# Kernel tuning notes

Hardware: AMD Instinct MI355X
Metric: run time of the kernel (lower is better)

## Reference

```python
import jax, jax.numpy as jnp
import numpy as np

B, S, D, H = 2, 2048, 1024, 16
DK = D // H  # 64
THETA = 10000.0


def setup_inputs() -> dict:
    key = jax.random.key(0)
    ks = jax.random.split(key, 5)
    std = float(np.sqrt(2.0 / (D + D)))
    x = jax.random.normal(ks[0], (B, S, D), dtype=jnp.float32)
    q_proj = jax.random.normal(ks[1], (D, D), dtype=jnp.float32) * std
    k_proj = jax.random.normal(ks[2], (D, D), dtype=jnp.float32) * std
    v_proj = jax.random.normal(ks[3], (D, D), dtype=jnp.float32) * std
    o_proj = jax.random.normal(ks[4], (D, D), dtype=jnp.float32) * std
    token_positions = jnp.arange(S, dtype=jnp.int32).reshape(1, S)
    return {"x": x, "token_positions": token_positions,
            "q_proj": q_proj, "k_proj": k_proj, "v_proj": v_proj, "o_proj": o_proj}


def _rope(t, pos):
    # t: [B, H, S, DK]; pos: [S]. Equivalent to multiplying by the block-diagonal
    # rotation matrix R[pos] in the source (interleaved 2x2 rotations).
    inv_freq = 1.0 / (THETA ** (2.0 * jnp.arange(DK // 2, dtype=jnp.float32) / DK))
    ang = pos.astype(jnp.float32)[:, None] * inv_freq[None, :]  # [S, DK/2]
    c, s = jnp.cos(ang), jnp.sin(ang)
    t0, t1 = t[..., 0::2], t[..., 1::2]
    out0 = c * t0 - s * t1
    out1 = s * t0 + c * t1
    return jnp.stack([out0, out1], axis=-1).reshape(t.shape)


def reference(x, token_positions, q_proj, k_proj, v_proj, o_proj):
    def split_heads(t):  # [B,S,D] -> [B,H,S,DK]
        return t.reshape(B, S, H, DK).transpose(0, 2, 1, 3)

    q = split_heads(jnp.einsum('bsd,ed->bse', x, q_proj))
    k = split_heads(jnp.einsum('bsd,ed->bse', x, k_proj))
    v = split_heads(jnp.einsum('bsd,ed->bse', x, v_proj))

    pos = token_positions[0]
    q = _rope(q, pos)
    k = _rope(k, pos)

    scores = jnp.einsum('bhqd,bhkd->bhqk', q, k) / jnp.sqrt(jnp.float32(DK))
    causal = jnp.tril(jnp.ones((S, S), dtype=bool))
    scores = jnp.where(causal, scores, -jnp.inf)

    # Faithful to source softmax: subtract the GLOBAL max (x.max()), then row-normalize.
    p = jnp.exp(scores - jnp.max(scores))
    p = p / jnp.sum(p, axis=-1, keepdims=True)

    attn = jnp.einsum('bhqk,bhkd->bhqd', p, v)
    attn = attn.transpose(0, 2, 1, 3).reshape(B, S, D)  # merge heads
    return jnp.einsum('bsd,ed->bse', attn, o_proj)
```

## Files before the change

kernel.cpp:

```cpp
#include <hip/hip_runtime.h>
#include <math.h>

#define B_  2
#define S_  2048
#define D_  1024
#define H_  16
#define DK_ 64
#define M_  (B_ * S_)

using u16 = unsigned short;
using u32 = unsigned int;
typedef __attribute__((ext_vector_type(8))) short  short8;
typedef __attribute__((ext_vector_type(4))) short  short4v;
typedef __attribute__((ext_vector_type(4))) float  float4v;
typedef __attribute__((ext_vector_type(4))) float  f32x4;

__device__ __forceinline__ float bf2f(u16 h) {
  u32 u = ((u32)h) << 16;
  return __builtin_bit_cast(float, u);
}
__device__ __forceinline__ u16 f2bf(float f) {
  u32 u = __builtin_bit_cast(u32, f);
  u32 r = u + 0x7fffu + ((u >> 16) & 1u);
  return (u16)(r >> 16);
}
__device__ __forceinline__ u16 f2bf_fast(float f) {
  u32 u = __builtin_bit_cast(u32, f);
  return (u16)((u + 0x8000u) >> 16);
}

__device__ __forceinline__ void async16(const void* g, void* l) {
  __builtin_amdgcn_global_load_lds((const __attribute__((address_space(1))) void*)g,
                                   (__attribute__((address_space(3))) void*)l,
                                   16, 0, 0);
}

#define MFMA16(a, b, c) __builtin_amdgcn_mfma_f32_16x16x32_bf16((a), (b), (c), 0, 0, 0)

__device__ __forceinline__ void stc(u16* p, float v)   { *p = f2bf(v); }
__device__ __forceinline__ void stc(float* p, float v) { *p = v; }

#define XG_ (M_ * D_ / 4)
#define WG_ (D_ * D_ / 4)
__global__ __launch_bounds__(256) void cvt5_kernel(
    const float* __restrict__ x,  const float* __restrict__ wq,
    const float* __restrict__ wk, const float* __restrict__ wv,
    const float* __restrict__ wo, u16* __restrict__ Xb, u16* __restrict__ Wqb,
    u16* __restrict__ Wkb, u16* __restrict__ Wvb, u16* __restrict__ Wob) {
  int i = blockIdx.x * 256 + threadIdx.x;
  const float* s; u16* d; int off;
  if (i < XG_)                { s = x;  d = Xb;  off = i; }
  else if (i < XG_ + WG_)     { s = wq; d = Wqb; off = i - XG_; }
  else if (i < XG_ + 2 * WG_) { s = wk; d = Wkb; off = i - XG_ - WG_; }
  else if (i < XG_ + 3 * WG_) { s = wv; d = Wvb; off = i - XG_ - 2 * WG_; }
  else                        { s = wo; d = Wob; off = i - XG_ - 3 * WG_; }
  f32x4 v = ((const f32x4*)s)[off];
  short4v o;
  o[0] = (short)f2bf(v[0]); o[1] = (short)f2bf(v[1]);
  o[2] = (short)f2bf(v[2]); o[3] = (short)f2bf(v[3]);
  ((short4v*)d)[off] = o;
}

template <typename TC>
__device__ __forceinline__ void gemm_tile(const u16* __restrict__ A,
                                          const u16* __restrict__ Bw,
                                          TC* __restrict__ C,
                                          int K, int N, int m0, int n0) {
  __shared__ __align__(16) u16 As[128 * 32];
  __shared__ __align__(16) u16 Bs[128 * 32];
  const int tid  = threadIdx.x;
  const int lane = tid & 63;
  const int wave = tid >> 6;
  const int quad = lane >> 4;
  const int l15  = lane & 15;
  const int wm   = (wave >> 1) << 6;
  const int wn   = (wave & 1) << 6;

  float4v acc[4][4];
#pragma unroll
  for (int i = 0; i < 4; ++i)
#pragma unroll
    for (int j = 0; j < 4; ++j) acc[i][j] = (float4v){0.f, 0.f, 0.f, 0.f};

  for (int k0 = 0; k0 < K; k0 += 32) {
#pragma unroll
    for (int i = 0; i < 2; ++i) {
      const int cbase = i * 256 + wave * 64;
      const int c     = cbase + lane;
      async16(A  + (size_t)(m0 + (c >> 2)) * K + k0 + ((c & 3) << 3), As + cbase * 8);
      async16(Bw + (size_t)(n0 + (c >> 2)) * K + k0 + ((c & 3) << 3), Bs + cbase * 8);
    }
    __syncthreads();

    short8 af[4], bfr[4];
#pragma unroll
    for (int mi = 0; mi < 4; ++mi)
      af[mi] = *(const short8*)(As + (wm + mi * 16 + l15) * 32 + quad * 8);
#pragma unroll
    for (int ni = 0; ni < 4; ++ni)
      bfr[ni] = *(const short8*)(Bs + (wn + ni * 16 + l15) * 32 + quad * 8);
#pragma unroll
    for (int mi = 0; mi < 4; ++mi)
#pragma unroll
      for (int ni = 0; ni < 4; ++ni)
        acc[mi][ni] = MFMA16(af[mi], bfr[ni], acc[mi][ni]);
    __syncthreads();
  }

#pragma unroll
  for (int mi = 0; mi < 4; ++mi)
#pragma unroll
    for (int ni = 0; ni < 4; ++ni)
#pragma unroll
      for (int r = 0; r < 4; ++r) {
        const int row = m0 + wm + mi * 16 + quad * 4 + r;
        const int col = n0 + wn + ni * 16 + l15;
        stc(C + (size_t)row * N + col, acc[mi][ni][r]);
      }
}

__global__ __launch_bounds__(256) void gemm_qkv_kernel(
    const u16* __restrict__ X, const u16* __restrict__ Wq,
    const u16* __restrict__ Wk, const u16* __restrict__ Wv,
    u16* Qb, u16* Kb, u16* Vb) {
  const int mt  = blockIdx.x;
  const int nn  = blockIdx.y;
  const int sel = nn >> 3;
  const int nt  = nn & 7;
  const u16* Bw = (sel == 0) ? Wq : (sel == 1) ? Wk : Wv;
  u16*       C  = (sel == 0) ? Qb : (sel == 1) ? Kb : Vb;
  gemm_tile(X, Bw, C, D_, D_, mt * 128, nt * 128);
}

__global__ __launch_bounds__(256) void gemm_o_kernel(
    const u16* __restrict__ Ab, const u16* __restrict__ Wo, float* Out) {
  gemm_tile(Ab, Wo, Out, D_, D_, blockIdx.x * 128, blockIdx.y * 128);
}

__global__ void rope_kernel(u16* __restrict__ Qb, u16* __restrict__ Kb,
                            const void* __restrict__ posv) {
  const int idx = blockIdx.x * 256 + threadIdx.x;
  const int i = idx & 31;
  const int h = (idx >> 5) & (H_ - 1);
  const int s = (idx >> 9) & (S_ - 1);
  const int b = idx >> 20;
  const int* p32 = (const int*)posv;
  const bool is64 = (p32[1] == 0 && p32[2] == 1);
  const int  ps   = is64 ? p32[2 * s] : p32[s];
  const float p    = (float)ps;
  const float freq = exp2f(-0.4152410118609203f * (float)i);
  float sn, cs;
  sincosf(p * freq, &sn, &cs);
  const size_t base = (size_t)(b * S_ + s) * D_ + h * DK_ + 2 * i;
  const float q0v = bf2f(Qb[base]), q1v = bf2f(Qb[base + 1]);
  Qb[base]     = f2bf(0.125f * (cs * q0v - sn * q1v));
  Qb[base + 1] = f2bf(0.125f * (sn * q0v + cs * q1v));
  const float k0v = bf2f(Kb[base]), k1v = bf2f(Kb[base + 1]);
  Kb[base]     = f2bf(cs * k0v - sn * k1v);
  Kb[base + 1] = f2bf(sn * k0v + cs * k1v);
}

__global__ __launch_bounds__(256) void vtrans_kernel(const u16* __restrict__ Vb,
                                                     u16* __restrict__ Vt) {
  const int sblk = blockIdx.x;
  const int bh   = blockIdx.y;
  const int b = bh >> 4, h = bh & 15;
  const int t = threadIdx.x;
  const int s0 = sblk * 64;
  __shared__ __align__(16) u16 T[64 * 72];

  {
    const int srow = t >> 2;
    const int dseg = (t & 3) << 4;
    const u16* g = Vb + (size_t)(b * S_ + s0 + srow) * D_ + h * DK_ + dseg;
    *(short8*)(T + srow * 72 + dseg)     = *(const short8*)(g);
    *(short8*)(T + srow * 72 + dseg + 8) = *(const short8*)(g + 8);
  }
  __syncthreads();
  {
    const int dk   = t >> 2;
    const int sseg = (t & 3) << 4;
    short8 o0, o1;
#pragma unroll
    for (int j = 0; j < 8; ++j) {
      o0[j] = (short)T[(sseg + j) * 72 + dk];
      o1[j] = (short)T[(sseg + 8 + j) * 72 + dk];
    }
    u16* g = Vt + (size_t)(bh * DK_ + dk) * S_ + s0 + sseg;
    *(short8*)(g)     = o0;
    *(short8*)(g + 8) = o1;
  }
}

__global__ __launch_bounds__(128) void attn_kernel(const u16* __restrict__ Qb,
                                                   const u16* __restrict__ Kb,
                                                   const u16* __restrict__ Vt,
                                                   u16* __restrict__ Ob) {
  const int qt = (blockIdx.x + blockIdx.y) & 31;
  const int bh = blockIdx.y;
  const int b = bh >> 4, h = bh & 15;
  const int tid = threadIdx.x, lane = tid & 63, wave = tid >> 6;
  const int quad = lane >> 4, l15 = lane & 15;
  const int qw = qt * 64 + wave * 32;

  __shared__ __align__(16) u16 Ks[2][64 * 64];
  __shared__ __align__(16) u16 Vs[2][64 * 64];

  const u16* Kbh = Kb + (size_t)b * S_ * D_ + h * DK_;
  const u16* Vbh = Vt + (size_t)bh * DK_ * S_;

  auto stage = [&](int kt, int bsel) {
    const int k0 = kt * 64;
#pragma unroll
    for (int i = 0; i < 4; ++i) {
      const int cb  = i * 128 + wave * 64;
      const int c   = cb + lane;
      const int row = c >> 3;
      const int gch = (c & 7) ^ (row & 7);
      async16(Kbh + (size_t)(k0 + row) * D_ + gch * 8, &Ks[bsel][cb * 8]);
      async16(Vbh + (size_t)row * S_ + k0 + gch * 8, &Vs[bsel][cb * 8]);
    }
  };

  short8 qf[2][2];
#pragma unroll
  for (int rg = 0; rg < 2; ++rg) {
    const u16* qrow = Qb + (size_t)(b * S_ + qw + rg * 16 + l15) * D_ + h * DK_;
    qf[rg][0] = *(const short8*)(qrow + quad * 8);
    qf[rg][1] = *(const short8*)(qrow + 32 + quad * 8);
  }

  float4v oacc[2][4];
#pragma unroll
  for (int rg = 0; rg < 2; ++rg)
#pragma unroll
    for (int n2 = 0; n2 < 4; ++n2) oacc[rg][n2] = (float4v){0.f, 0.f, 0.f, 0.f};
  float lsum0 = 0.f, lsum1 = 0.f;

  stage(0, 0);

  for (int kt = 0; kt <= qt; ++kt) {
    const int bsel = kt & 1;
    __syncthreads();
    if (kt < qt) stage(kt + 1, bsel ^ 1);

    const u16* ks = Ks[bsel];
    const u16* vs = Vs[bsel];

    float4v sc[2][4];
#pragma unroll
    for (int ni = 0; ni < 4; ++ni) {
      const int kr = ni * 16 + l15;
      const int x  = kr & 7;
      const short8 kf0 = *(const short8*)(ks + kr * 64 + ((quad ^ x) << 3));
      const short8 kf1 = *(const short8*)(ks + kr * 64 + (((quad | 4) ^ x) << 3));
      float4v z = (float4v){0.f, 0.f, 0.f, 0.f};
      sc[0][ni] = MFMA16(kf1, qf[0][1], MFMA16(kf0, qf[0][0], z));
      sc[1][ni] = MFMA16(kf1, qf[1][1], MFMA16(kf0, qf[1][0], z));
    }

    const int k0 = kt * 64;
    if (kt == qt) {
#pragma unroll
      for (int rg = 0; rg < 2; ++rg) {
        const int qr = qw + rg * 16 + l15;
#pragma unroll
        for (int ni = 0; ni < 4; ++ni)
#pragma unroll
          for (int r = 0; r < 4; ++r) {
            const float e = __expf(sc[rg][ni][r]);
            sc[rg][ni][r] = (k0 + ni * 16 + quad * 4 + r > qr) ? 0.f : e;
          }
      }
    } else {
#pragma unroll
      for (int rg = 0; rg < 2; ++rg)
#pragma unroll
        for (int ni = 0; ni < 4; ++ni)
#pragma unroll
          for (int r = 0; r < 4; ++r) sc[rg][ni][r] = __expf(sc[rg][ni][r]);
    }

    short8 pfr[2][2];
#pragma unroll
    for (int rg = 0; rg < 2; ++rg)
#pragma unroll
      for (int s = 0; s < 2; ++s) {
        short8 pf;
#pragma unroll
        for (int r = 0; r < 4; ++r) {
          pf[r]     = (short)f2bf_fast(sc[rg][2 * s][r]);
          pf[r + 4] = (short)f2bf_fast(sc[rg][2 * s + 1][r]);
        }
        pfr[rg][s] = pf;
      }
#pragma unroll
    for (int ni = 0; ni < 4; ++ni)
#pragma unroll
      for (int r = 0; r < 4; ++r) {
        lsum0 += sc[0][ni][r];
        lsum1 += sc[1][ni][r];
      }

#pragma unroll
    for (int s = 0; s < 2; ++s)
#pragma unroll
      for (int n2 = 0; n2 < 4; ++n2) {
        const int vr = n2 * 16 + l15;
        const int x  = vr & 7;
        const int cl = (((s << 2) | (quad >> 1)) ^ x);
        const int ch = (((s << 2) | 2 | (quad >> 1)) ^ x);
        const int hb = (quad & 1) << 2;
        short4v vlo = *(const short4v*)(vs + vr * 64 + (cl << 3) + hb);
        short4v vhi = *(const short4v*)(vs + vr * 64 + (ch << 3) + hb);
        short8 vf;
#pragma unroll
        for (int e = 0; e < 4; ++e) { vf[e] = vlo[e]; vf[e + 4] = vhi[e]; }
        oacc[0][n2] = MFMA16(pfr[0][s], vf, oacc[0][n2]);
        oacc[1][n2] = MFMA16(pfr[1][s], vf, oacc[1][n2]);
      }
  }

  float ls[2] = {lsum0, lsum1};
#pragma unroll
  for (int rg = 0; rg < 2; ++rg) {
    float t = ls[rg];
    t += __shfl_xor(t, 16, 64);
    t += __shfl_xor(t, 32, 64);
    float rinv[4];
#pragma unroll
    for (int r = 0; r < 4; ++r) rinv[r] = 1.0f / __shfl(t, quad * 4 + r, 64);
#pragma unroll
    for (int n2 = 0; n2 < 4; ++n2)
#pragma unroll
      for (int r = 0; r < 4; ++r) {
        const int srow = qw + rg * 16 + quad * 4 + r;
        Ob[(size_t)(b * S_ + srow) * D_ + h * DK_ + n2 * 16 + l15] =
            f2bf(oacc[rg][n2][r] * rinv[r]);
      }
  }
}

extern "C" void kernel_launch(void* const* d_in, const int* in_sizes, int n_in,
                              void* d_out, int out_size, void* d_ws, size_t ws_size,
                              hipStream_t stream) {
  const float* x  = (const float*)d_in[0];
  const void*  tp = d_in[1];
  const float* wq = (const float*)d_in[2];
  const float* wk = (const float*)d_in[3];
  const float* wv = (const float*)d_in[4];
  const float* wo = (const float*)d_in[5];
  float* out = (float*)d_out;

  u16* Qb  = (u16*)d_ws;
  u16* Kb  = Qb + (size_t)M_ * D_;
  u16* Vb  = Kb + (size_t)M_ * D_;
  u16* Vt  = Vb + (size_t)M_ * D_;
  u16* Ab  = Vt + (size_t)M_ * D_;
  u16* Xb  = Ab;
  u16* Wqb = Ab + (size_t)M_ * D_;
  u16* Wkb = Wqb + (size_t)D_ * D_;
  u16* Wvb = Wkb + (size_t)D_ * D_;
  u16* Wob = Wvb + (size_t)D_ * D_;

  cvt5_kernel<<<dim3((XG_ + 4 * WG_) / 256), dim3(256), 0, stream>>>(
      x, wq, wk, wv, wo, Xb, Wqb, Wkb, Wvb, Wob);
  gemm_qkv_kernel<<<dim3(32, 24), dim3(256), 0, stream>>>(Xb, Wqb, Wkb, Wvb, Qb, Kb, Vb);
  rope_kernel<<<dim3((B_ * S_ * H_ * 32) / 256), dim3(256), 0, stream>>>(Qb, Kb, tp);
  vtrans_kernel<<<dim3(32, 32), dim3(256), 0, stream>>>(Vb, Vt);
  attn_kernel<<<dim3(32, 32), dim3(128), 0, stream>>>(Qb, Kb, Vt, Ab);
  gemm_o_kernel<<<dim3(32, 8), dim3(256), 0, stream>>>(Ab, Wob, out);
}
```

Before: 211.9 us.

## Deepen attention K/V pipeline with half-tiles, vectorize RoPE, reorder query tiles

The attention kernel now streams K/V in 32-key half-tiles through a 4-slot LDS ring with three loads in flight and explicit vmcnt waits instead of a double buffer with __syncthreads. It also sets wave priority around the MFMA sections, packs probabilities with v_cvt_pk_bf16_f32, and remaps query tiles so short and long causal rows are interleaved. The RoPE kernel processes 8 elements per thread with 16-byte loads and stores instead of scalar accesses. The aim is to hide load latency and cut conversion and memory-instruction overhead. In exchange, the kernel uses hand-written waitcnt counts that must match the number of issued loads, and each half-tile does fewer MFMAs per barrier.

```diff
diff --git a/kernel.cpp b/kernel.cpp
--- a/kernel.cpp
+++ b/kernel.cpp
@@ -14,6 +14,7 @@
 typedef __attribute__((ext_vector_type(4))) short  short4v;
 typedef __attribute__((ext_vector_type(4))) float  float4v;
 typedef __attribute__((ext_vector_type(4))) float  f32x4;
+typedef __attribute__((ext_vector_type(4))) u32    u32x4;
 
 __device__ __forceinline__ float bf2f(u16 h) {
   u32 u = ((u32)h) << 16;
@@ -23,10 +24,6 @@
   u32 u = __builtin_bit_cast(u32, f);
   u32 r = u + 0x7fffu + ((u >> 16) & 1u);
   return (u16)(r >> 16);
-}
-__device__ __forceinline__ u16 f2bf_fast(float f) {
-  u32 u = __builtin_bit_cast(u32, f);
-  return (u16)((u + 0x8000u) >> 16);
 }
 
 __device__ __forceinline__ void async16(const void* g, void* l) {
@@ -137,27 +134,37 @@
   gemm_tile(Ab, Wo, Out, D_, D_, blockIdx.x * 128, blockIdx.y * 128);
 }
 
-__global__ void rope_kernel(u16* __restrict__ Qb, u16* __restrict__ Kb,
-                            const void* __restrict__ posv) {
-  const int idx = blockIdx.x * 256 + threadIdx.x;
-  const int i = idx & 31;
-  const int h = (idx >> 5) & (H_ - 1);
-  const int s = (idx >> 9) & (S_ - 1);
-  const int b = idx >> 20;
+__global__ __launch_bounds__(256) void rope_kernel(u16* __restrict__ Qb,
+                                                   u16* __restrict__ Kb,
+                                                   const void* __restrict__ posv) {
+  const int t  = blockIdx.x * 256 + threadIdx.x;
+  const int p4 = t & 7;
+  const int h  = (t >> 3) & (H_ - 1);
+  const int s  = (t >> 7) & (S_ - 1);
+  const int b  = t >> 18;
   const int* p32 = (const int*)posv;
   const bool is64 = (p32[1] == 0 && p32[2] == 1);
   const int  ps   = is64 ? p32[2 * s] : p32[s];
-  const float p    = (float)ps;
-  const float freq = exp2f(-0.4152410118609203f * (float)i);
-  float sn, cs;
-  sincosf(p * freq, &sn, &cs);
-  const size_t base = (size_t)(b * S_ + s) * D_ + h * DK_ + 2 * i;
-  const float q0v = bf2f(Qb[base]), q1v = bf2f(Qb[base + 1]);
-  Qb[base]     = f2bf(0.125f * (cs * q0v - sn * q1v));
-  Qb[base + 1] = f2bf(0.125f * (sn * q0v + cs * q1v));
-  const float k0v = bf2f(Kb[base]), k1v = bf2f(Kb[base + 1]);
-  Kb[base]     = f2bf(cs * k0v - sn * k1v);
-  Kb[base + 1] = f2bf(sn * k0v + cs * k1v);
+  const float p   = (float)ps;
+  const size_t base = (size_t)(b * S_ + s) * D_ + h * DK_ + p4 * 8;
+  short8 qv = *(const short8*)(Qb + base);
+  short8 kv = *(const short8*)(Kb + base);
+  short8 qo, ko;
+#pragma unroll
+  for (int j = 0; j < 4; ++j) {
+    const int i = p4 * 4 + j;
+    const float freq = exp2f(-0.4152410118609203f * (float)i);
+    float sn, cs;
+    sincosf(p * freq, &sn, &cs);
+    const float q0v = bf2f((u16)qv[2 * j]), q1v = bf2f((u16)qv[2 * j + 1]);
+    qo[2 * j]     = (short)f2bf(0.125f * (cs * q0v - sn * q1v));
+    qo[2 * j + 1] = (short)f2bf(0.125f * (sn * q0v + cs * q1v));
+    const float k0v = bf2f((u16)kv[2 * j]), k1v = bf2f((u16)kv[2 * j + 1]);
+    ko[2 * j]     = (short)f2bf(cs * k0v - sn * k1v);
+    ko[2 * j + 1] = (short)f2bf(sn * k0v + cs * k1v);
+  }
+  *(short8*)(Qb + base) = qo;
+  *(short8*)(Kb + base) = ko;
 }
 
 __global__ __launch_bounds__(256) void vtrans_kernel(const u16* __restrict__ Vb,
@@ -196,29 +203,39 @@
                                                    const u16* __restrict__ Kb,
                                                    const u16* __restrict__ Vt,
                                                    u16* __restrict__ Ob) {
-  const int qt = (blockIdx.x + blockIdx.y) & 31;
+  const int j5 = (blockIdx.x + blockIdx.y) & 31;
+  const int r5 = j5 & 7, g5 = j5 >> 3;
+  const int qt = (g5 == 0) ? r5 : (g5 == 1) ? r5 + 8 : (g5 == 2) ? 23 - r5 : 31 - r5;
   const int bh = blockIdx.y;
   const int b = bh >> 4, h = bh & 15;
   const int tid = threadIdx.x, lane = tid & 63, wave = tid >> 6;
   const int quad = lane >> 4, l15 = lane & 15;
   const int qw = qt * 64 + wave * 32;
 
-  __shared__ __align__(16) u16 Ks[2][64 * 64];
-  __shared__ __align__(16) u16 Vs[2][64 * 64];
+  __shared__ __align__(16) u16 Kh[4][32 * 64];
+  __shared__ __align__(16) u16 Vh[4][64 * 32];
 
   const u16* Kbh = Kb + (size_t)b * S_ * D_ + h * DK_;
   const u16* Vbh = Vt + (size_t)bh * DK_ * S_;
 
-  auto stage = [&](int kt, int bsel) {
-    const int k0 = kt * 64;
-#pragma unroll
-    for (int i = 0; i < 4; ++i) {
-      const int cb  = i * 128 + wave * 64;
+  auto stage = [&](int j) {
+    const int sel = j & 3;
+    const int k0  = j * 32;
+#pragma unroll
+    for (int i = 0; i < 2; ++i) {
+      const int cb  = wave * 128 + i * 64;
       const int c   = cb + lane;
       const int row = c >> 3;
-      const int gch = (c & 7) ^ (row & 7);
-      async16(Kbh + (size_t)(k0 + row) * D_ + gch * 8, &Ks[bsel][cb * 8]);
-      async16(Vbh + (size_t)row * S_ + k0 + gch * 8, &Vs[bsel][cb * 8]);
+      const int ch  = (c & 7) ^ (row & 7);
+      async16(Kbh + (size_t)(k0 + row) * D_ + ch * 8, &Kh[sel][cb * 8]);
+    }
+#pragma unroll
+    for (int i = 0; i < 2; ++i) {
+      const int cb = wave * 128 + i * 64;
+      const int c  = cb + lane;
+      const int rv = c >> 2;
+      const int ch = (c & 3) ^ ((rv >> 1) & 3);
+      async16(Vbh + (size_t)rv * S_ + k0 + ch * 8, &Vh[sel][cb * 8]);
     }
   };
 
@@ -237,19 +254,27 @@
     for (int n2 = 0; n2 < 4; ++n2) oacc[rg][n2] = (float4v){0.f, 0.f, 0.f, 0.f};
   float lsum0 = 0.f, lsum1 = 0.f;
 
-  stage(0, 0);
-
-  for (int kt = 0; kt <= qt; ++kt) {
-    const int bsel = kt & 1;
-    __syncthreads();
-    if (kt < qt) stage(kt + 1, bsel ^ 1);
-
-    const u16* ks = Ks[bsel];
-    const u16* vs = Vs[bsel];
-
-    float4v sc[2][4];
-#pragma unroll
-    for (int ni = 0; ni < 4; ++ni) {
+  const int NS = 2 * qt + 2;
+  stage(0);
+  stage(1);
+  if (NS > 2) stage(2);
+
+  for (int hs = 0; hs < NS; ++hs) {
+    if (hs + 2 < NS)      asm volatile("s_waitcnt vmcnt(8)" ::: "memory");
+    else if (hs + 1 < NS) asm volatile("s_waitcnt vmcnt(4)" ::: "memory");
+    else                  asm volatile("s_waitcnt vmcnt(0)" ::: "memory");
+    __builtin_amdgcn_s_barrier();
+    asm volatile("" ::: "memory");
+    if (hs + 3 < NS) stage(hs + 3);
+
+    const int sel = hs & 3;
+    const u16* ks = Kh[sel];
+    const u16* vs = Vh[sel];
+
+    float4v sc[2][2];
+    __builtin_amdgcn_s_setprio(1);
+#pragma unroll
+    for (int ni = 0; ni < 2; ++ni) {
       const int kr = ni * 16 + l15;
       const int x  = kr & 7;
       const short8 kf0 = *(const short8*)(ks + kr * 64 + ((quad ^ x) << 3));
@@ -258,67 +283,63 @@
       sc[0][ni] = MFMA16(kf1, qf[0][1], MFMA16(kf0, qf[0][0], z));
       sc[1][ni] = MFMA16(kf1, qf[1][1], MFMA16(kf0, qf[1][0], z));
     }
-
-    const int k0 = kt * 64;
-    if (kt == qt) {
+    __builtin_amdgcn_s_setprio(0);
+
+    const int kbase = hs * 32;
+    if (kbase + 31 > qw) {
 #pragma unroll
       for (int rg = 0; rg < 2; ++rg) {
         const int qr = qw + rg * 16 + l15;
 #pragma unroll
-        for (int ni = 0; ni < 4; ++ni)
+        for (int ni = 0; ni < 2; ++ni)
 #pragma unroll
           for (int r = 0; r < 4; ++r) {
             const float e = __expf(sc[rg][ni][r]);
-            sc[rg][ni][r] = (k0 + ni * 16 + quad * 4 + r > qr) ? 0.f : e;
+            sc[rg][ni][r] = (kbase + ni * 16 + quad * 4 + r > qr) ? 0.f : e;
           }
       }
     } else {
 #pragma unroll
       for (int rg = 0; rg < 2; ++rg)
 #pragma unroll
-        for (int ni = 0; ni < 4; ++ni)
+        for (int ni = 0; ni < 2; ++ni)
 #pragma unroll
           for (int r = 0; r < 4; ++r) sc[rg][ni][r] = __expf(sc[rg][ni][r]);
     }
 
-    short8 pfr[2][2];
-#pragma unroll
-    for (int rg = 0; rg < 2; ++rg)
-#pragma unroll
-      for (int s = 0; s < 2; ++s) {
-        short8 pf;
-#pragma unroll
-        for (int r = 0; r < 4; ++r) {
-          pf[r]     = (short)f2bf_fast(sc[rg][2 * s][r]);
-          pf[r + 4] = (short)f2bf_fast(sc[rg][2 * s + 1][r]);
-        }
-        pfr[rg][s] = pf;
-      }
-#pragma unroll
-    for (int ni = 0; ni < 4; ++ni)
+    short8 pfr[2];
+#pragma unroll
+    for (int rg = 0; rg < 2; ++rg) {
+      u32 w0, w1, w2, w3;
+      asm("v_cvt_pk_bf16_f32 %0, %1, %2" : "=v"(w0) : "v"(sc[rg][0][0]), "v"(sc[rg][0][1]));
+      asm("v_cvt_pk_bf16_f32 %0, %1, %2" : "=v"(w1) : "v"(sc[rg][0][2]), "v"(sc[rg][0][3]));
+      asm("v_cvt_pk_bf16_f32 %0, %1, %2" : "=v"(w2) : "v"(sc[rg][1][0]), "v"(sc[rg][1][1]));
+      asm("v_cvt_pk_bf16_f32 %0, %1, %2" : "=v"(w3) : "v"(sc[rg][1][2]), "v"(sc[rg][1][3]));
+      u32x4 ww = (u32x4){w0, w1, w2, w3};
+      pfr[rg] = __builtin_bit_cast(short8, ww);
+    }
+#pragma unroll
+    for (int ni = 0; ni < 2; ++ni)
 #pragma unroll
       for (int r = 0; r < 4; ++r) {
         lsum0 += sc[0][ni][r];
         lsum1 += sc[1][ni][r];
       }
 
-#pragma unroll
-    for (int s = 0; s < 2; ++s)
-#pragma unroll
-      for (int n2 = 0; n2 < 4; ++n2) {
-        const int vr = n2 * 16 + l15;
-        const int x  = vr & 7;
-        const int cl = (((s << 2) | (quad >> 1)) ^ x);
-        const int ch = (((s << 2) | 2 | (quad >> 1)) ^ x);
-        const int hb = (quad & 1) << 2;
-        short4v vlo = *(const short4v*)(vs + vr * 64 + (cl << 3) + hb);
-        short4v vhi = *(const short4v*)(vs + vr * 64 + (ch << 3) + hb);
-        short8 vf;
-#pragma unroll
-        for (int e = 0; e < 4; ++e) { vf[e] = vlo[e]; vf[e + 4] = vhi[e]; }
-        oacc[0][n2] = MFMA16(pfr[0][s], vf, oacc[0][n2]);
-        oacc[1][n2] = MFMA16(pfr[1][s], vf, oacc[1][n2]);
-      }
+    __builtin_amdgcn_s_setprio(1);
+#pragma unroll
+    for (int n2 = 0; n2 < 4; ++n2) {
+      const int vr = n2 * 16 + l15;
+      const int sw = (vr >> 1) & 3;
+      const short4v vlo = *(const short4v*)(vs + vr * 32 + (((quad >> 1) ^ sw) << 3) + ((quad & 1) << 2));
+      const short4v vhi = *(const short4v*)(vs + vr * 32 + (((2 | (quad >> 1)) ^ sw) << 3) + ((quad & 1) << 2));
+      short8 vf;
+#pragma unroll
+      for (int e = 0; e < 4; ++e) { vf[e] = vlo[e]; vf[e + 4] = vhi[e]; }
+      oacc[0][n2] = MFMA16(pfr[0], vf, oacc[0][n2]);
+      oacc[1][n2] = MFMA16(pfr[1], vf, oacc[1][n2]);
+    }
+    __builtin_amdgcn_s_setprio(0);
   }
 
   float ls[2] = {lsum0, lsum1};
@@ -366,7 +387,7 @@
   cvt5_kernel<<<dim3((XG_ + 4 * WG_) / 256), dim3(256), 0, stream>>>(
       x, wq, wk, wv, wo, Xb, Wqb, Wkb, Wvb, Wob);
   gemm_qkv_kernel<<<dim3(32, 24), dim3(256), 0, stream>>>(Xb, Wqb, Wkb, Wvb, Qb, Kb, Vb);
-  rope_kernel<<<dim3((B_ * S_ * H_ * 32) / 256), dim3(256), 0, stream>>>(Qb, Kb, tp);
+  rope_kernel<<<dim3((B_ * S_ * H_ * 8) / 256), dim3(256), 0, stream>>>(Qb, Kb, tp);
   vtrans_kernel<<<dim3(32, 32), dim3(256), 0, stream>>>(Vb, Vt);
   attn_kernel<<<dim3(32, 32), dim3(128), 0, stream>>>(Qb, Kb, Vt, Ab);
   gemm_o_kernel<<<dim3(32, 8), dim3(256), 0, stream>>>(Ab, Wob, out);
```

Result: no change. 214.4 us (+1.2%).
